# Optimization experiments

Measured on AMD Instinct MI355X. Metric: run time of the kernel, lower is better.

Reference implementation:

```python
import jax, jax.numpy as jnp
import numpy as np

HEAD_NUM = 6

def setup_inputs() -> dict:
    key = jax.random.key(0)
    k1, k2, k3 = jax.random.split(key, 3)
    B, N, P, C = 4, 64, 256, 384
    x = jax.random.normal(k1, (B, N, P, C), dtype=jnp.float32)
    # torch Linear init scale ~ 1/sqrt(fan_in); keep magnitudes sane
    w_qkv = jax.random.normal(k2, (C, 3 * C), dtype=jnp.float32) * (1.0 / np.sqrt(C))
    w_proj = jax.random.normal(k3, (C, C), dtype=jnp.float32) * (1.0 / np.sqrt(C))
    b_proj = jnp.zeros((C,), dtype=jnp.float32)
    return {"x": x, "w_qkv": w_qkv, "w_proj": w_proj, "b_proj": b_proj}

def reference(x, w_qkv, w_proj, b_proj):
    B, N, P, C = x.shape
    H = HEAD_NUM
    D = C // H
    scale = jnp.asarray(D, dtype=x.dtype)  # NOTE: head_dim ** 1, faithful to source
    qkv = (x @ w_qkv).reshape(B, N, P, 3, H, D)
    q = qkv[:, :, :, 0]  # (B, N, P, H, D)
    k = qkv[:, :, :, 1]
    v = qkv[:, :, :, 2]
    attn = jnp.einsum('bnphd,bnqhd->bnhpq', q, k) * scale  # (B,N,H,P,P)
    attn = jax.nn.softmax(attn, axis=-1)
    out = jnp.einsum('bnhpq,bnqhd->bnphd', attn, v).reshape(B, N, P, C)
    return out @ w_proj + b_proj
```

## Files before the change

### kernel.cpp

```cpp
#include <hip/hip_runtime.h>

typedef __bf16 bf16_t;
typedef __bf16 bf16x8 __attribute__((ext_vector_type(8)));
typedef float f32x4 __attribute__((ext_vector_type(4)));
typedef unsigned short u16;
typedef unsigned short u16x4 __attribute__((ext_vector_type(4)));
typedef unsigned int u32;

#define B_ 4
#define N_ 64
#define P_ 256
#define C_ 384
#define H_ 6
#define D_ 64
#define M_TOTAL 65536
#define NQKV 1152
#define KSTEPS 12
#define NBLK (H_*B_*N_)
#define WKS_U16 10240
#define WKS_BYTES 20480
#define FUSED_LDS 139264
#define PB_STRIDE 40
#define SB() __builtin_amdgcn_sched_barrier(0)

#define GLOAD_LDS16(g, l) __builtin_amdgcn_global_load_lds( \
    (const __attribute__((address_space(1))) void*)(g), \
    (__attribute__((address_space(3))) void*)(l), 16, 0, 0)

__device__ __forceinline__ u16 f2b(float f){ return __builtin_bit_cast(u16, (bf16_t)f); }
__device__ __forceinline__ f32x4 mfma(bf16x8 a, bf16x8 b, f32x4 c){
    return __builtin_amdgcn_mfma_f32_16x16x32_bf16(a, b, c, 0, 0, 0);
}

__global__ __launch_bounds__(256) void prep_w(
    const float* __restrict__ wqkv, const float* __restrict__ wproj,
    u16* __restrict__ Wpk, u16* __restrict__ wPt)
{
    int i = blockIdx.x * 256 + threadIdx.x;
    const int NSLOT = H_ * KSTEPS * 12 * 64;
    if (i < NSLOT) {
        int lane = i & 63;
        int frag = i >> 6;
        int nf = frag % 12;
        int ks = (frag / 12) % KSTEPS;
        int h  = frag / (12 * KSTEPS);
        int part = nf >> 2;
        int nh   = (nf & 3) * 16 + (lane & 15);
        int col  = part * C_ + h * 64 + nh;
        int k0   = ks * 32 + (lane >> 4) * 8;
        size_t base = (size_t)(h * KSTEPS + ks) * WKS_U16;
        #pragma unroll
        for (int e = 0; e < 8; ++e) {
            float w = wqkv[(size_t)(k0 + e) * NQKV + col];
            bf16_t hi = (bf16_t)w;
            Wpk[base + nf * 512 + lane * 8 + e] = __builtin_bit_cast(u16, hi);
            if (nf < 8)
                Wpk[base + 6144 + nf * 512 + lane * 8 + e] = f2b(w - (float)hi);
        }
    }
    int j = i - NSLOT;
    if (j >= 0 && j < C_ * C_) {
        int k = j / C_, n = j % C_;
        wPt[(size_t)n * C_ + k] = f2b(wproj[j]);
    }
}

__global__ __launch_bounds__(1024, 4) void fused_attn(
    const float* __restrict__ x, const u16* __restrict__ Wpk,
    u16* __restrict__ attn)
{
    extern __shared__ u16 sm[];
    u16* Kh = sm;
    u16* Kl = sm + 16384;
    u16* Vt = sm + 32768;

    const int tid  = threadIdx.x;
    const int lane = tid & 63, wid = tid >> 6;
    const int g = lane >> 4, r16 = lane & 15;

    const int p = blockIdx.x;
    const int logical = (p & 7) * (NBLK / 8) + (p >> 3);
    const int h  = logical % H_;
    const int bn = logical / H_;
    const size_t row0 = (size_t)bn * P_;
    const int m0w = wid * 16;

    f32x4 acc[12];
    #pragma unroll
    for (int nf = 0; nf < 12; ++nf) acc[nf] = f32x4{0.f,0.f,0.f,0.f};

    const float* xr0 = x + (row0 + m0w + r16) * C_;
    const char* wbase = (const char*)Wpk + (size_t)h * (KSTEPS * WKS_BYTES);

#define STAGE(ks_, par_) do { \
    const char* _gp = wbase + (size_t)(ks_) * WKS_BYTES; \
    char* _lp = (char*)(sm + 49152 + (par_) * WKS_U16); \
    GLOAD_LDS16(_gp + tid * 16, _lp + tid * 16); \
    if (tid < 256) GLOAD_LDS16(_gp + 16384 + tid * 16, _lp + 16384 + tid * 16); \
} while (0)

    f32x4 xr[2][2];
#define XLOAD(ks_, par_) do { \
    const float* _xp = xr0 + (ks_) * 32 + 8 * g; \
    xr[par_][0] = *(const f32x4*)_xp; xr[par_][1] = *(const f32x4*)(_xp + 4); \
} while (0)

    bf16x8 ah, al;
#define SPLIT_A(par_) do { \
    _Pragma("unroll") \
    for (int e = 0; e < 4; ++e) { \
        bf16_t h0 = (bf16_t)xr[par_][0][e], h1 = (bf16_t)xr[par_][1][e]; \
        ah[e]   = h0; al[e]   = (bf16_t)(xr[par_][0][e] - (float)h0); \
        ah[4+e] = h1; al[4+e] = (bf16_t)(xr[par_][1][e] - (float)h1); \
    } } while (0)

    STAGE(0, 0);
    XLOAD(0, 0);
    __syncthreads();

    #pragma unroll
    for (int ks = 0; ks < KSTEPS; ++ks) {
        const int par = ks & 1, nxt = par ^ 1;
        if (ks < KSTEPS - 1) {
            STAGE(ks + 1, nxt);
            XLOAD(ks + 1, nxt);
        }
        SPLIT_A(par);
        const u16* stg = sm + 49152 + par * WKS_U16;
        #pragma unroll
        for (int nf = 0; nf < 8; ++nf) {
            bf16x8 bh = *(const bf16x8*)&stg[nf * 512 + lane * 8];
            bf16x8 bl = *(const bf16x8*)&stg[6144 + nf * 512 + lane * 8];
            acc[nf] = mfma(ah, bh, acc[nf]);
            acc[nf] = mfma(ah, bl, acc[nf]);
            acc[nf] = mfma(al, bh, acc[nf]);
        }
        #pragma unroll
        for (int nf = 8; nf < 12; ++nf) {
            bf16x8 bh = *(const bf16x8*)&stg[nf * 512 + lane * 8];
            acc[nf] = mfma(ah, bh, acc[nf]);
        }
        __syncthreads();
    }

    #pragma unroll
    for (int f = 0; f < 4; ++f)
    #pragma unroll
    for (int rr = 0; rr < 4; ++rr) {
        int q = m0w + 4 * g + rr;
        int d = f * 16 + r16;
        int ek = q * 64 + (((d >> 3) ^ (q & 7)) << 3) + (d & 7);
        float kv = acc[4 + f][rr];
        bf16_t khi = (bf16_t)kv;
        Kh[ek] = __builtin_bit_cast(u16, khi);
        Kl[ek] = f2b(kv - (float)khi);
        Vt[d * 256 + (((q >> 3) ^ (d & 7)) << 3) + (q & 7)] = f2b(acc[8 + f][rr]);
    }

    u16* myQb = sm + 49152 + wid * 1024;
    bf16x8 aqh[2], aql[2];
    #pragma unroll
    for (int f = 0; f < 4; ++f)
    #pragma unroll
    for (int rr = 0; rr < 4; ++rr) {
        int r = 4 * g + rr;
        int c = f * 16 + r16;
        myQb[r * 64 + (((c >> 3) ^ (r & 7)) << 3) + (c & 7)] = f2b(acc[f][rr]);
    }
    #pragma unroll
    for (int k2 = 0; k2 < 2; ++k2)
        aqh[k2] = *(const bf16x8*)&myQb[r16 * 64 + (((k2 * 4 + g) ^ (r16 & 7)) << 3)];
    SB();
    #pragma unroll
    for (int f = 0; f < 4; ++f)
    #pragma unroll
    for (int rr = 0; rr < 4; ++rr) {
        int r = 4 * g + rr;
        int c = f * 16 + r16;
        float v = acc[f][rr];
        bf16_t hi = (bf16_t)v;
        myQb[r * 64 + (((c >> 3) ^ (r & 7)) << 3) + (c & 7)] = f2b(v - (float)hi);
    }
    #pragma unroll
    for (int k2 = 0; k2 < 2; ++k2)
        aql[k2] = *(const bf16x8*)&myQb[r16 * 64 + (((k2 * 4 + g) ^ (r16 & 7)) << 3)];

    __syncthreads();

    f32x4 S[16];
    #pragma unroll
    for (int nf = 0; nf < 16; ++nf) S[nf] = f32x4{0.f,0.f,0.f,0.f};

    bf16x8 khv[2][2], klv[2][2];
    {
        int q = r16;
        #pragma unroll
        for (int k2 = 0; k2 < 2; ++k2) {
            int e = q * 64 + (((k2 * 4 + g) ^ (q & 7)) << 3);
            khv[0][k2] = *(const bf16x8*)&Kh[e];
            klv[0][k2] = *(const bf16x8*)&Kl[e];
        }
    }
    #pragma unroll
    for (int nf = 0; nf < 16; ++nf) {
        const int par = nf & 1, nxt = par ^ 1;
        if (nf < 15) {
            int q = (nf + 1) * 16 + r16;
            #pragma unroll
            for (int k2 = 0; k2 < 2; ++k2) {
                int e = q * 64 + (((k2 * 4 + g) ^ (q & 7)) << 3);
                khv[nxt][k2] = *(const bf16x8*)&Kh[e];
                klv[nxt][k2] = *(const bf16x8*)&Kl[e];
            }
        }
        SB();
        __builtin_amdgcn_s_setprio(1);
        #pragma unroll
        for (int k2 = 0; k2 < 2; ++k2) {
            S[nf] = mfma(aqh[k2], khv[par][k2], S[nf]);
            S[nf] = mfma(aqh[k2], klv[par][k2], S[nf]);
            S[nf] = mfma(aql[k2], khv[par][k2], S[nf]);
        }
        __builtin_amdgcn_s_setprio(0);
        SB();
    }

    {
        float mrow[4] = {-1e30f,-1e30f,-1e30f,-1e30f};
        #pragma unroll
        for (int nf = 0; nf < 16; ++nf)
            #pragma unroll
            for (int rr = 0; rr < 4; ++rr) mrow[rr] = fmaxf(mrow[rr], S[nf][rr]);
        #pragma unroll
        for (int mask = 1; mask < 16; mask <<= 1)
            #pragma unroll
            for (int rr = 0; rr < 4; ++rr) mrow[rr] = fmaxf(mrow[rr], __shfl_xor(mrow[rr], mask, 64));
        float ssum[4] = {0.f,0.f,0.f,0.f};
        #pragma unroll
        for (int nf = 0; nf < 16; ++nf)
            #pragma unroll
            for (int rr = 0; rr < 4; ++rr) {
                float pv = __expf((S[nf][rr] - mrow[rr]) * 64.0f);
                S[nf][rr] = pv;
                ssum[rr] += pv;
            }
        #pragma unroll
        for (int mask = 1; mask < 16; mask <<= 1)
            #pragma unroll
            for (int rr = 0; rr < 4; ++rr) ssum[rr] += __shfl_xor(ssum[rr], mask, 64);
        float inv_[4];
        #pragma unroll
        for (int rr = 0; rr < 4; ++rr) inv_[rr] = 1.0f / ssum[rr];
        #pragma unroll
        for (int nf = 0; nf < 16; ++nf)
            #pragma unroll
            for (int rr = 0; rr < 4; ++rr) S[nf][rr] *= inv_[rr];
    }

    f32x4 O[4];
    #pragma unroll
    for (int f = 0; f < 4; ++f) O[f] = f32x4{0.f,0.f,0.f,0.f};

    u16* pb = sm + 49152 + wid * 640;
    #pragma unroll
    for (int t = 0; t < 8; ++t) {
        bf16x8 bv[4];
        #pragma unroll
        for (int f = 0; f < 4; ++f) {
            int d = f * 16 + r16;
            bv[f] = *(const bf16x8*)&Vt[d * 256 + ((((t * 32 + 8 * g) >> 3) ^ (d & 7)) << 3)];
        }
        #pragma unroll
        for (int tt = 0; tt < 2; ++tt) {
            int nf = 2 * t + tt;
            #pragma unroll
            for (int rr = 0; rr < 4; ++rr)
                pb[(4 * g + rr) * PB_STRIDE + tt * 16 + r16] = f2b(S[nf][rr]);
        }
        bf16x8 ap = *(const bf16x8*)&pb[r16 * PB_STRIDE + 8 * g];
        __builtin_amdgcn_s_setprio(1);
        #pragma unroll
        for (int f = 0; f < 4; ++f) O[f] = mfma(ap, bv[f], O[f]);
        __builtin_amdgcn_s_setprio(0);
    }

    #pragma unroll
    for (int f = 0; f < 4; ++f)
    #pragma unroll
    for (int rr = 0; rr < 4; ++rr)
        attn[(row0 + m0w + 4 * g + rr) * C_ + h * 64 + f * 16 + r16] = f2b(O[f][rr]);
}

__global__ __launch_bounds__(256, 2) void proj_kernel(
    const u16* __restrict__ attn, const u16* __restrict__ wPt,
    const float* __restrict__ bias, float* __restrict__ out)
{
    __shared__ alignas(16) u16 As[128*32];
    __shared__ alignas(16) u16 Bs[128*32];

    const int tid = threadIdx.x;
    const int lane = tid & 63, wid = tid >> 6;
    const int wr = wid >> 1, wc = wid & 1;
    const int g = lane >> 4, r16 = lane & 15;
    const int m0 = blockIdx.x * 128;
    const int n0 = blockIdx.y * 128;

    f32x4 acc[4][4];
    for (int i = 0; i < 4; i++) for (int j = 0; j < 4; j++) acc[i][j] = f32x4{0.f,0.f,0.f,0.f};

    for (int kt = 0; kt < C_; kt += 32) {
        for (int r = 0; r < 4; ++r) {
            int i = tid + 256*r;
            int mm = i >> 3;
            int kk = (i & 7) << 2;
            u16x4 v = *(const u16x4*)&attn[(size_t)(m0+mm)*C_ + kt + kk];
            int e = mm*32 + (((kk>>3) ^ ((mm>>1)&3))<<3) + (kk&7);
            *(u16x4*)&As[e] = v;
        }
        for (int r = 0; r < 4; ++r) {
            int i = tid + 256*r;
            int nn = i >> 3;
            int kk = (i & 7) << 2;
            u16x4 v = *(const u16x4*)&wPt[(size_t)(n0+nn)*C_ + kt + kk];
            int e = nn*32 + (((kk>>3) ^ ((nn>>1)&3))<<3) + (kk&7);
            *(u16x4*)&Bs[e] = v;
        }
        __syncthreads();

        bf16x8 a[4], b[4];
        for (int i = 0; i < 4; i++) {
            int row = wr*64 + i*16 + r16;
            a[i] = *(const bf16x8*)&As[row*32 + ((g ^ ((row>>1)&3))<<3)];
        }
        for (int j = 0; j < 4; j++) {
            int n = wc*64 + j*16 + r16;
            b[j] = *(const bf16x8*)&Bs[n*32 + ((g ^ ((n>>1)&3))<<3)];
        }
        for (int i = 0; i < 4; i++) for (int j = 0; j < 4; j++)
            acc[i][j] = mfma(a[i], b[j], acc[i][j]);
        __syncthreads();
    }

    for (int i = 0; i < 4; i++) for (int j = 0; j < 4; j++) for (int rr = 0; rr < 4; rr++) {
        size_t row = m0 + wr*64 + i*16 + g*4 + rr;
        int col = n0 + wc*64 + j*16 + r16;
        out[row*C_ + col] = acc[i][j][rr] + bias[col];
    }
}

extern "C" void kernel_launch(void* const* d_in, const int* in_sizes, int n_in,
                              void* d_out, int out_size, void* d_ws, size_t ws_size,
                              hipStream_t stream)
{
    const float* x      = (const float*)d_in[0];
    const float* w_qkv  = (const float*)d_in[1];
    const float* w_proj = (const float*)d_in[2];
    const float* b_proj = (const float*)d_in[3];
    float* out = (float*)d_out;

    u16* ws = (u16*)d_ws;
    u16* attnb = ws;
    size_t off = (size_t)M_TOTAL * C_;
    u16* Wpk = ws + off; off += (size_t)H_ * KSTEPS * WKS_U16;
    u16* wPt = ws + off; off += (size_t)C_ * C_;

    hipFuncSetAttribute((const void*)fused_attn,
                        hipFuncAttributeMaxDynamicSharedMemorySize, FUSED_LDS);

    int prep_n = H_ * KSTEPS * 12 * 64 + C_ * C_;
    prep_w<<<dim3((prep_n + 255) / 256), 256, 0, stream>>>(w_qkv, w_proj, Wpk, wPt);
    fused_attn<<<dim3(NBLK), 1024, FUSED_LDS, stream>>>(x, Wpk, attnb);
    proj_kernel<<<dim3(M_TOTAL / 128, C_ / 128), 256, 0, stream>>>(attnb, wPt, b_proj, out);
}
```

Before: 248.6 us.

## Retile QKV projection into 32-row by half-column warp tiles with shared weight fragments

The QKV GEMM inside the fused attention kernel is re-tiled. Each wave now computes 32 rows by half of the head's columns instead of 16 rows by all columns, so each LDS weight fragment feeds two MFMAs and LDS reads per MFMA are halved. The weight packing is reordered into two column groups to match, and Q is now staged through a shared LDS buffer with extra block-wide barriers so each wave can gather its own 16 rows for the attention phase. The trade-off is that x rows are loaded by two waves each, and the added __syncthreads calls may cost time.

```diff
diff --git a/kernel.cpp b/kernel.cpp
--- a/kernel.cpp
+++ b/kernel.cpp
@@ -37,25 +37,27 @@
     u16* __restrict__ Wpk, u16* __restrict__ wPt)
 {
     int i = blockIdx.x * 256 + threadIdx.x;
-    const int NSLOT = H_ * KSTEPS * 12 * 64;
+    const int NSLOT = H_ * KSTEPS * 20 * 64;
     if (i < NSLOT) {
         int lane = i & 63;
         int frag = i >> 6;
-        int nf = frag % 12;
-        int ks = (frag / 12) % KSTEPS;
-        int h  = frag / (12 * KSTEPS);
-        int part = nf >> 2;
-        int nh   = (nf & 3) * 16 + (lane & 15);
-        int col  = part * C_ + h * 64 + nh;
+        int fi = frag % 20;
+        int ks = (frag / 20) % KSTEPS;
+        int h  = frag / (20 * KSTEPS);
+        int cg = fi / 10;
+        int f  = fi % 10;
+        int isLo = (f >= 6);
+        int j  = isLo ? f - 6 : f;
+        int part = j >> 1;
+        int jj   = j & 1;
+        int col  = part * C_ + h * 64 + (cg * 2 + jj) * 16 + (lane & 15);
         int k0   = ks * 32 + (lane >> 4) * 8;
-        size_t base = (size_t)(h * KSTEPS + ks) * WKS_U16;
         #pragma unroll
         for (int e = 0; e < 8; ++e) {
             float w = wqkv[(size_t)(k0 + e) * NQKV + col];
             bf16_t hi = (bf16_t)w;
-            Wpk[base + nf * 512 + lane * 8 + e] = __builtin_bit_cast(u16, hi);
-            if (nf < 8)
-                Wpk[base + 6144 + nf * 512 + lane * 8 + e] = f2b(w - (float)hi);
+            Wpk[(size_t)i * 8 + e] = isLo ? f2b(w - (float)hi)
+                                          : __builtin_bit_cast(u16, hi);
         }
     }
     int j = i - NSLOT;
@@ -73,6 +75,7 @@
     u16* Kh = sm;
     u16* Kl = sm + 16384;
     u16* Vt = sm + 32768;
+    u16* Qx = sm + 49152;
 
     const int tid  = threadIdx.x;
     const int lane = tid & 63, wid = tid >> 6;
@@ -83,13 +86,19 @@
     const int h  = logical % H_;
     const int bn = logical / H_;
     const size_t row0 = (size_t)bn * P_;
-    const int m0w = wid * 16;
-
-    f32x4 acc[12];
-    #pragma unroll
-    for (int nf = 0; nf < 12; ++nf) acc[nf] = f32x4{0.f,0.f,0.f,0.f};
-
-    const float* xr0 = x + (row0 + m0w + r16) * C_;
+
+    const int rg = wid >> 1;
+    const int cg = wid & 1;
+    const int m0w1 = rg * 32;
+
+    f32x4 acc[2][6];
+    #pragma unroll
+    for (int mf = 0; mf < 2; ++mf)
+        #pragma unroll
+        for (int j = 0; j < 6; ++j) acc[mf][j] = f32x4{0.f,0.f,0.f,0.f};
+
+    const float* xr0 = x + (row0 + m0w1 + r16) * C_;
+    const float* xr1 = xr0 + 16 * C_;
     const char* wbase = (const char*)Wpk + (size_t)h * (KSTEPS * WKS_BYTES);
 
 #define STAGE(ks_, par_) do { \
@@ -99,92 +108,95 @@
     if (tid < 256) GLOAD_LDS16(_gp + 16384 + tid * 16, _lp + 16384 + tid * 16); \
 } while (0)
 
-    f32x4 xr[2][2];
-#define XLOAD(ks_, par_) do { \
-    const float* _xp = xr0 + (ks_) * 32 + 8 * g; \
-    xr[par_][0] = *(const f32x4*)_xp; xr[par_][1] = *(const f32x4*)(_xp + 4); \
-} while (0)
-
-    bf16x8 ah, al;
-#define SPLIT_A(par_) do { \
-    _Pragma("unroll") \
-    for (int e = 0; e < 4; ++e) { \
-        bf16_t h0 = (bf16_t)xr[par_][0][e], h1 = (bf16_t)xr[par_][1][e]; \
-        ah[e]   = h0; al[e]   = (bf16_t)(xr[par_][0][e] - (float)h0); \
-        ah[4+e] = h1; al[4+e] = (bf16_t)(xr[par_][1][e] - (float)h1); \
-    } } while (0)
-
     STAGE(0, 0);
-    XLOAD(0, 0);
     __syncthreads();
 
     #pragma unroll
     for (int ks = 0; ks < KSTEPS; ++ks) {
         const int par = ks & 1, nxt = par ^ 1;
-        if (ks < KSTEPS - 1) {
-            STAGE(ks + 1, nxt);
-            XLOAD(ks + 1, nxt);
-        }
-        SPLIT_A(par);
-        const u16* stg = sm + 49152 + par * WKS_U16;
-        #pragma unroll
-        for (int nf = 0; nf < 8; ++nf) {
-            bf16x8 bh = *(const bf16x8*)&stg[nf * 512 + lane * 8];
-            bf16x8 bl = *(const bf16x8*)&stg[6144 + nf * 512 + lane * 8];
-            acc[nf] = mfma(ah, bh, acc[nf]);
-            acc[nf] = mfma(ah, bl, acc[nf]);
-            acc[nf] = mfma(al, bh, acc[nf]);
-        }
-        #pragma unroll
-        for (int nf = 8; nf < 12; ++nf) {
-            bf16x8 bh = *(const bf16x8*)&stg[nf * 512 + lane * 8];
-            acc[nf] = mfma(ah, bh, acc[nf]);
+        if (ks < KSTEPS - 1) STAGE(ks + 1, nxt);
+
+        f32x4 xa0 = *(const f32x4*)(xr0 + ks * 32 + 8 * g);
+        f32x4 xa1 = *(const f32x4*)(xr0 + ks * 32 + 8 * g + 4);
+        f32x4 xb0 = *(const f32x4*)(xr1 + ks * 32 + 8 * g);
+        f32x4 xb1 = *(const f32x4*)(xr1 + ks * 32 + 8 * g + 4);
+        bf16x8 ah[2], al[2];
+        #pragma unroll
+        for (int e = 0; e < 4; ++e) {
+            bf16_t h0 = (bf16_t)xa0[e], h1 = (bf16_t)xa1[e];
+            ah[0][e]   = h0; al[0][e]   = (bf16_t)(xa0[e] - (float)h0);
+            ah[0][4+e] = h1; al[0][4+e] = (bf16_t)(xa1[e] - (float)h1);
+            bf16_t h2 = (bf16_t)xb0[e], h3 = (bf16_t)xb1[e];
+            ah[1][e]   = h2; al[1][e]   = (bf16_t)(xb0[e] - (float)h2);
+            ah[1][4+e] = h3; al[1][4+e] = (bf16_t)(xb1[e] - (float)h3);
+        }
+
+        const u16* cgb = sm + 49152 + par * WKS_U16 + cg * 5120;
+        #pragma unroll
+        for (int j = 0; j < 4; ++j) {
+            bf16x8 bh = *(const bf16x8*)&cgb[j * 512 + lane * 8];
+            bf16x8 bl = *(const bf16x8*)&cgb[(6 + j) * 512 + lane * 8];
+            #pragma unroll
+            for (int mf = 0; mf < 2; ++mf) {
+                acc[mf][j] = mfma(ah[mf], bh, acc[mf][j]);
+                acc[mf][j] = mfma(ah[mf], bl, acc[mf][j]);
+                acc[mf][j] = mfma(al[mf], bh, acc[mf][j]);
+            }
+        }
+        #pragma unroll
+        for (int j = 4; j < 6; ++j) {
+            bf16x8 bh = *(const bf16x8*)&cgb[j * 512 + lane * 8];
+            #pragma unroll
+            for (int mf = 0; mf < 2; ++mf)
+                acc[mf][j] = mfma(ah[mf], bh, acc[mf][j]);
         }
         __syncthreads();
     }
 
     #pragma unroll
-    for (int f = 0; f < 4; ++f)
+    for (int mf = 0; mf < 2; ++mf)
+    #pragma unroll
+    for (int jj = 0; jj < 2; ++jj)
     #pragma unroll
     for (int rr = 0; rr < 4; ++rr) {
-        int q = m0w + 4 * g + rr;
-        int d = f * 16 + r16;
+        int q = m0w1 + mf * 16 + 4 * g + rr;
+        int d = (cg * 2 + jj) * 16 + r16;
         int ek = q * 64 + (((d >> 3) ^ (q & 7)) << 3) + (d & 7);
-        float kv = acc[4 + f][rr];
+        float kv = acc[mf][2 + jj][rr];
         bf16_t khi = (bf16_t)kv;
         Kh[ek] = __builtin_bit_cast(u16, khi);
         Kl[ek] = f2b(kv - (float)khi);
-        Vt[d * 256 + (((q >> 3) ^ (d & 7)) << 3) + (q & 7)] = f2b(acc[8 + f][rr]);
-    }
-
-    u16* myQb = sm + 49152 + wid * 1024;
+        Vt[d * 256 + (((q >> 3) ^ (d & 7)) << 3) + (q & 7)] = f2b(acc[mf][4 + jj][rr]);
+        Qx[ek] = f2b(acc[mf][jj][rr]);
+    }
+    __syncthreads();
+
+    const int m0w = wid * 16;
     bf16x8 aqh[2], aql[2];
     #pragma unroll
-    for (int f = 0; f < 4; ++f)
+    for (int k2 = 0; k2 < 2; ++k2) {
+        int q = m0w + r16;
+        aqh[k2] = *(const bf16x8*)&Qx[q * 64 + (((k2 * 4 + g) ^ (q & 7)) << 3)];
+    }
+    __syncthreads();
+    #pragma unroll
+    for (int mf = 0; mf < 2; ++mf)
+    #pragma unroll
+    for (int jj = 0; jj < 2; ++jj)
     #pragma unroll
     for (int rr = 0; rr < 4; ++rr) {
-        int r = 4 * g + rr;
-        int c = f * 16 + r16;
-        myQb[r * 64 + (((c >> 3) ^ (r & 7)) << 3) + (c & 7)] = f2b(acc[f][rr]);
-    }
-    #pragma unroll
-    for (int k2 = 0; k2 < 2; ++k2)
-        aqh[k2] = *(const bf16x8*)&myQb[r16 * 64 + (((k2 * 4 + g) ^ (r16 & 7)) << 3)];
-    SB();
-    #pragma unroll
-    for (int f = 0; f < 4; ++f)
-    #pragma unroll
-    for (int rr = 0; rr < 4; ++rr) {
-        int r = 4 * g + rr;
-        int c = f * 16 + r16;
-        float v = acc[f][rr];
+        int q = m0w1 + mf * 16 + 4 * g + rr;
+        int d = (cg * 2 + jj) * 16 + r16;
+        float v = acc[mf][jj][rr];
         bf16_t hi = (bf16_t)v;
-        myQb[r * 64 + (((c >> 3) ^ (r & 7)) << 3) + (c & 7)] = f2b(v - (float)hi);
-    }
-    #pragma unroll
-    for (int k2 = 0; k2 < 2; ++k2)
-        aql[k2] = *(const bf16x8*)&myQb[r16 * 64 + (((k2 * 4 + g) ^ (r16 & 7)) << 3)];
-
+        Qx[q * 64 + (((d >> 3) ^ (q & 7)) << 3) + (d & 7)] = f2b(v - (float)hi);
+    }
+    __syncthreads();
+    #pragma unroll
+    for (int k2 = 0; k2 < 2; ++k2) {
+        int q = m0w + r16;
+        aql[k2] = *(const bf16x8*)&Qx[q * 64 + (((k2 * 4 + g) ^ (q & 7)) << 3)];
+    }
     __syncthreads();
 
     f32x4 S[16];
@@ -367,7 +379,7 @@
     hipFuncSetAttribute((const void*)fused_attn,
                         hipFuncAttributeMaxDynamicSharedMemorySize, FUSED_LDS);
 
-    int prep_n = H_ * KSTEPS * 12 * 64 + C_ * C_;
+    int prep_n = H_ * KSTEPS * 20 * 64 + C_ * C_;
     prep_w<<<dim3((prep_n + 255) / 256), 256, 0, stream>>>(w_qkv, w_proj, Wpk, wPt);
     fused_attn<<<dim3(NBLK), 1024, FUSED_LDS, stream>>>(x, Wpk, attnb);
     proj_kernel<<<dim3(M_TOTAL / 128, C_ / 128), 256, 0, stream>>>(attnb, wPt, b_proj, out);
```

Result: slower. 308.3 us (+24.0%).

## Triple-buffer weight staging with vmcnt waits and vectorize V stores

Applied to the files above, without the earlier changes.

Moves the QKV weight staging to three LDS buffers at the start of shared memory, prefetching two k-steps ahead and replacing the per-step __syncthreads with explicit vmcnt waits plus s_barrier. This is meant to hide global-to-LDS latency better and drop the full barrier drain. The tail of each stage now goes through 4-byte global_load_lds, which lets every thread issue its load without a branch. Other changes: V-transpose stores become 4-wide u16 vector stores, and K/V address arithmetic is hoisted. LDS shrinks, which may raise occupancy, but the buffers now overlap the region later reused for K/V/Q, and the hand-written vmcnt counts depend on the number of outstanding loads.

```diff
diff --git a/kernel.cpp b/kernel.cpp
--- a/kernel.cpp
+++ b/kernel.cpp
@@ -19,13 +19,16 @@
 #define NBLK (H_*B_*N_)
 #define WKS_U16 10240
 #define WKS_BYTES 20480
-#define FUSED_LDS 139264
+#define FUSED_LDS 131072
 #define PB_STRIDE 40
 #define SB() __builtin_amdgcn_sched_barrier(0)
 
 #define GLOAD_LDS16(g, l) __builtin_amdgcn_global_load_lds( \
     (const __attribute__((address_space(1))) void*)(g), \
     (__attribute__((address_space(3))) void*)(l), 16, 0, 0)
+#define GLOAD_LDS4(g, l) __builtin_amdgcn_global_load_lds( \
+    (const __attribute__((address_space(1))) void*)(g), \
+    (__attribute__((address_space(3))) void*)(l), 4, 0, 0)
 
 __device__ __forceinline__ u16 f2b(float f){ return __builtin_bit_cast(u16, (bf16_t)f); }
 __device__ __forceinline__ f32x4 mfma(bf16x8 a, bf16x8 b, f32x4 c){
@@ -92,11 +95,11 @@
     const float* xr0 = x + (row0 + m0w + r16) * C_;
     const char* wbase = (const char*)Wpk + (size_t)h * (KSTEPS * WKS_BYTES);
 
-#define STAGE(ks_, par_) do { \
+#define STAGE(ks_, b_) do { \
     const char* _gp = wbase + (size_t)(ks_) * WKS_BYTES; \
-    char* _lp = (char*)(sm + 49152 + (par_) * WKS_U16); \
+    char* _lp = (char*)(sm + (b_) * WKS_U16); \
     GLOAD_LDS16(_gp + tid * 16, _lp + tid * 16); \
-    if (tid < 256) GLOAD_LDS16(_gp + 16384 + tid * 16, _lp + 16384 + tid * 16); \
+    GLOAD_LDS4(_gp + 16384 + tid * 4, _lp + 16384 + tid * 4); \
 } while (0)
 
     f32x4 xr[2][2];
@@ -116,17 +119,20 @@
 
     STAGE(0, 0);
     XLOAD(0, 0);
-    __syncthreads();
+    STAGE(1, 1);
+    SB();
+    asm volatile("s_waitcnt vmcnt(2)" ::: "memory");
+    __builtin_amdgcn_s_barrier();
+    SB();
 
     #pragma unroll
     for (int ks = 0; ks < KSTEPS; ++ks) {
         const int par = ks & 1, nxt = par ^ 1;
-        if (ks < KSTEPS - 1) {
-            STAGE(ks + 1, nxt);
-            XLOAD(ks + 1, nxt);
-        }
+        if (ks + 2 < KSTEPS) STAGE(ks + 2, (ks + 2) % 3);
+        if (ks + 1 < KSTEPS) XLOAD(ks + 1, nxt);
         SPLIT_A(par);
-        const u16* stg = sm + 49152 + par * WKS_U16;
+
+        const u16* stg = sm + (ks % 3) * WKS_U16;
         #pragma unroll
         for (int nf = 0; nf < 8; ++nf) {
             bf16x8 bh = *(const bf16x8*)&stg[nf * 512 + lane * 8];
@@ -140,21 +146,35 @@
             bf16x8 bh = *(const bf16x8*)&stg[nf * 512 + lane * 8];
             acc[nf] = mfma(ah, bh, acc[nf]);
         }
-        __syncthreads();
-    }
-
-    #pragma unroll
-    for (int f = 0; f < 4; ++f)
-    #pragma unroll
-    for (int rr = 0; rr < 4; ++rr) {
-        int q = m0w + 4 * g + rr;
-        int d = f * 16 + r16;
-        int ek = q * 64 + (((d >> 3) ^ (q & 7)) << 3) + (d & 7);
-        float kv = acc[4 + f][rr];
-        bf16_t khi = (bf16_t)kv;
-        Kh[ek] = __builtin_bit_cast(u16, khi);
-        Kl[ek] = f2b(kv - (float)khi);
-        Vt[d * 256 + (((q >> 3) ^ (d & 7)) << 3) + (q & 7)] = f2b(acc[8 + f][rr]);
+
+        if (ks < KSTEPS - 1) {
+            SB();
+            if (ks + 2 < KSTEPS) asm volatile("s_waitcnt vmcnt(4)" ::: "memory");
+            else                 asm volatile("s_waitcnt vmcnt(2)" ::: "memory");
+            __builtin_amdgcn_s_barrier();
+            SB();
+        } else {
+            __syncthreads();
+        }
+    }
+
+    #pragma unroll
+    for (int f = 0; f < 4; ++f) {
+        const int d = f * 16 + r16;
+        const int q0 = m0w + 4 * g;
+        u16x4 vv;
+        #pragma unroll
+        for (int rr = 0; rr < 4; ++rr) vv[rr] = f2b(acc[8 + f][rr]);
+        *(u16x4*)&Vt[d * 256 + (((q0 >> 3) ^ (d & 7)) << 3) + (q0 & 7)] = vv;
+        #pragma unroll
+        for (int rr = 0; rr < 4; ++rr) {
+            int q = q0 + rr;
+            int ek = q * 64 + (((d >> 3) ^ (q & 7)) << 3) + (d & 7);
+            float kv = acc[4 + f][rr];
+            bf16_t khi = (bf16_t)kv;
+            Kh[ek] = __builtin_bit_cast(u16, khi);
+            Kl[ek] = f2b(kv - (float)khi);
+        }
     }
 
     u16* myQb = sm + 49152 + wid * 1024;
@@ -191,27 +211,25 @@
     #pragma unroll
     for (int nf = 0; nf < 16; ++nf) S[nf] = f32x4{0.f,0.f,0.f,0.f};
 
+    const int kb0 = r16 * 64 + (((0 * 4 + g) ^ (r16 & 7)) << 3);
+    const int kb1 = r16 * 64 + (((1 * 4 + g) ^ (r16 & 7)) << 3);
+
     bf16x8 khv[2][2], klv[2][2];
     {
-        int q = r16;
-        #pragma unroll
-        for (int k2 = 0; k2 < 2; ++k2) {
-            int e = q * 64 + (((k2 * 4 + g) ^ (q & 7)) << 3);
-            khv[0][k2] = *(const bf16x8*)&Kh[e];
-            klv[0][k2] = *(const bf16x8*)&Kl[e];
-        }
+        khv[0][0] = *(const bf16x8*)&Kh[kb0];
+        klv[0][0] = *(const bf16x8*)&Kl[kb0];
+        khv[0][1] = *(const bf16x8*)&Kh[kb1];
+        klv[0][1] = *(const bf16x8*)&Kl[kb1];
     }
     #pragma unroll
     for (int nf = 0; nf < 16; ++nf) {
         const int par = nf & 1, nxt = par ^ 1;
         if (nf < 15) {
-            int q = (nf + 1) * 16 + r16;
-            #pragma unroll
-            for (int k2 = 0; k2 < 2; ++k2) {
-                int e = q * 64 + (((k2 * 4 + g) ^ (q & 7)) << 3);
-                khv[nxt][k2] = *(const bf16x8*)&Kh[e];
-                klv[nxt][k2] = *(const bf16x8*)&Kl[e];
-            }
+            const int o = (nf + 1) * 1024;
+            khv[nxt][0] = *(const bf16x8*)&Kh[o + kb0];
+            klv[nxt][0] = *(const bf16x8*)&Kl[o + kb0];
+            khv[nxt][1] = *(const bf16x8*)&Kh[o + kb1];
+            klv[nxt][1] = *(const bf16x8*)&Kl[o + kb1];
         }
         SB();
         __builtin_amdgcn_s_setprio(1);
@@ -262,14 +280,14 @@
     for (int f = 0; f < 4; ++f) O[f] = f32x4{0.f,0.f,0.f,0.f};
 
     u16* pb = sm + 49152 + wid * 640;
+    const int vc = r16 & 7;
     #pragma unroll
     for (int t = 0; t < 8; ++t) {
         bf16x8 bv[4];
-        #pragma unroll
-        for (int f = 0; f < 4; ++f) {
-            int d = f * 16 + r16;
-            bv[f] = *(const bf16x8*)&Vt[d * 256 + ((((t * 32 + 8 * g) >> 3) ^ (d & 7)) << 3)];
-        }
+        const int vo = (((4 * t + g) ^ vc) << 3) + r16 * 256;
+        #pragma unroll
+        for (int f = 0; f < 4; ++f)
+            bv[f] = *(const bf16x8*)&Vt[f * 4096 + vo];
         #pragma unroll
         for (int tt = 0; tt < 2; ++tt) {
             int nf = 2 * t + tt;
```

New measurement: 243.8 us. About the same (-1.9%).
